# Performance work log

Measured on AMD Instinct MI355X. Metric: run time of the kernel, lower is better.

Reference implementation:

```python
import jax, jax.numpy as jnp
import numpy as np

N = 100000        # nodes
E = 3200000       # random edges (self-loops appended -> E + N total)
F_IN = 500        # in_channels
H = 32            # n_hidden (fixed in NormProp)
D = 64            # embedding_dim
K = 2             # propagation steps
LN_EPS = 1e-6


def setup_inputs() -> dict:
    key = jax.random.key(0)
    ks = jax.random.split(key, 6)
    x = jax.random.normal(ks[0], (N, F_IN), jnp.float32)
    src = jax.random.randint(ks[1], (E,), 0, N)
    dst = jax.random.randint(ks[2], (E,), 0, N)
    loop = jnp.arange(N)
    # edge_index already contains all self-loops, matching
    # add_remaining_self_loops' post-condition deterministically.
    edge_index = jnp.stack([jnp.concatenate([src, loop]),
                            jnp.concatenate([dst, loop])])
    W1 = jax.random.normal(ks[3], (F_IN, H), jnp.float32) * (1.0 / np.sqrt(F_IN))
    b1 = jnp.zeros((H,), jnp.float32)
    gamma = jnp.ones((H,), jnp.float32)
    beta = jnp.zeros((H,), jnp.float32)
    W2 = jax.random.normal(ks[4], (H, D), jnp.float32) * (1.0 / np.sqrt(H))
    b2 = jnp.zeros((D,), jnp.float32)
    return dict(x=x, edge_index=edge_index, W1=W1, b1=b1,
                gamma=gamma, beta=beta, W2=W2, b2=b2)


def reference(x, edge_index, W1, b1, gamma, beta, W2, b2):
    # Encoder (dropout p is inactive at eval): fc1 -> LayerNorm -> relu -> fc2
    h = x @ W1 + b1                                   # [N, H]
    mu = h.mean(-1, keepdims=True)
    var = ((h - mu) ** 2).mean(-1, keepdims=True)
    h = (h - mu) / jnp.sqrt(var + LN_EPS) * gamma + beta
    h = jax.nn.relu(h) @ W2 + b2                      # [N, D]
    # F.normalize(p=2, dim=-1) with eps=1e-12
    h = h / jnp.maximum(jnp.linalg.norm(h, axis=-1, keepdims=True), 1e-12)

    row, col = edge_index[0], edge_index[1]           # source -> target
    # gcn_norm: symmetric deg^{-1/2} normalization (edge_weight=None -> ones)
    deg = jax.ops.segment_sum(jnp.ones(row.shape, h.dtype), col, num_segments=N)
    dinv = jnp.where(deg > 0, jax.lax.rsqrt(deg), 0.0)
    norm = dinv[row] * dinv[col]                      # [E+N]

    hs = [h]
    for _ in range(K):
        # message: edge_weight * x_j ; aggregate: scatter-add into target
        h = jax.ops.segment_sum(norm[:, None] * h[row], col, num_segments=N)
        hs.append(h)
    return tuple(hs)
```

## Files before the change

kernel.cpp:

```cpp
#include <hip/hip_runtime.h>

#define F_IN 500
#define HH 32
#define DD 64
#define LN_EPS 1e-6f
#define QCAP 100000
#define SPAN 4096
#define FWN 448
#define FCAP 16384

typedef float f32x4 __attribute__((ext_vector_type(4)));
typedef _Float16 f16x8 __attribute__((ext_vector_type(8)));
typedef _Float16 f16x2 __attribute__((ext_vector_type(2)));
typedef _Float16 h16;

__global__ __launch_bounds__(256)
void prep_k(const float* __restrict__ W1, const float* __restrict__ W2,
            h16* __restrict__ w1t, h16* __restrict__ w2t)
{
    int i = blockIdx.x * 256 + threadIdx.x;
    if (i < 32 * 512) {
        int j = i >> 9, k = i & 511;
        w1t[i] = (k < F_IN) ? (h16)W1[k * HH + j] : (h16)0.f;
    }
    int i2 = i - 32 * 512;
    if (i2 >= 0 && i2 < 64 * 32) {
        int d = i2 >> 5, j = i2 & 31;
        w2t[i2] = (h16)W2[j * DD + d];
    }
}

__global__ __launch_bounds__(256)
void encoder_k(const float* __restrict__ x,
               const h16* __restrict__ w1t, const float* __restrict__ b1,
               const float* __restrict__ gamma, const float* __restrict__ beta,
               const h16* __restrict__ w2t, const float* __restrict__ b2,
               float* __restrict__ h0, int N)
{
    __shared__ h16 hbuf[4][512];

    const int t = threadIdx.x;
    const int w = t >> 6, l = t & 63;
    const int c0 = l & 15, kg = l >> 4;
    const int gr0 = (blockIdx.x * 4 + w) * 16;
    int rowA = gr0 + c0; if (rowA >= N) rowA = N - 1;
    const float* xr = x + (size_t)rowA * F_IN;

    float b1a = b1[c0], b1b = b1[c0 + 16];
    f32x4 acc0 = {b1a, b1a, b1a, b1a};
    f32x4 acc1 = {b1b, b1b, b1b, b1b};

    const h16* w1a = w1t + c0 * 512 + kg * 8;
    const h16* w1b = w1a + 16 * 512;

    #pragma unroll 3
    for (int ks = 0; ks < 15; ++ks) {
        const int k0 = ks * 32;
        f32x4 xa = *(const f32x4*)(xr + k0 + kg * 8);
        f32x4 xb = *(const f32x4*)(xr + k0 + kg * 8 + 4);
        f16x8 af;
        af[0] = (h16)xa[0]; af[1] = (h16)xa[1]; af[2] = (h16)xa[2]; af[3] = (h16)xa[3];
        af[4] = (h16)xb[0]; af[5] = (h16)xb[1]; af[6] = (h16)xb[2]; af[7] = (h16)xb[3];
        f16x8 bf0 = *(const f16x8*)(w1a + k0);
        f16x8 bf1 = *(const f16x8*)(w1b + k0);
        acc0 = __builtin_amdgcn_mfma_f32_16x16x32_f16(af, bf0, acc0, 0, 0, 0);
        acc1 = __builtin_amdgcn_mfma_f32_16x16x32_f16(af, bf1, acc1, 0, 0, 0);
    }
    {
        f16x8 af;
        #pragma unroll
        for (int e = 0; e < 8; ++e) {
            int k = 480 + kg * 8 + e;
            af[e] = (k < F_IN) ? (h16)xr[k] : (h16)0.f;
        }
        f16x8 bf0 = *(const f16x8*)(w1a + 480);
        f16x8 bf1 = *(const f16x8*)(w1b + 480);
        acc0 = __builtin_amdgcn_mfma_f32_16x16x32_f16(af, bf0, acc0, 0, 0, 0);
        acc1 = __builtin_amdgcn_mfma_f32_16x16x32_f16(af, bf1, acc1, 0, 0, 0);
    }

    float g0 = gamma[c0], g1 = gamma[c0 + 16];
    float be0 = beta[c0], be1 = beta[c0 + 16];
    h16* hb = hbuf[w];
    #pragma unroll
    for (int i = 0; i < 4; ++i) {
        float a0 = acc0[i], a1 = acc1[i];
        float s = a0 + a1;
        s += __shfl_xor(s, 1); s += __shfl_xor(s, 2);
        s += __shfl_xor(s, 4); s += __shfl_xor(s, 8);
        float mu = s * (1.0f / 32.0f);
        float d0 = a0 - mu, d1 = a1 - mu;
        float vv = d0 * d0 + d1 * d1;
        vv += __shfl_xor(vv, 1); vv += __shfl_xor(vv, 2);
        vv += __shfl_xor(vv, 4); vv += __shfl_xor(vv, 8);
        float is = rsqrtf(vv * (1.0f / 32.0f) + LN_EPS);
        float h0v = fmaxf(fmaf(d0 * is, g0, be0), 0.f);
        float h1v = fmaxf(fmaf(d1 * is, g1, be1), 0.f);
        int r = kg * 4 + i;
        hb[r * 32 + ((((c0 >> 3) ^ i) & 3) << 3) + (c0 & 7)] = (h16)h0v;
        hb[r * 32 + ((((2 + (c0 >> 3)) ^ i) & 3) << 3) + (c0 & 7)] = (h16)h1v;
    }
    asm volatile("s_waitcnt lgkmcnt(0)" ::: "memory");
    __builtin_amdgcn_sched_barrier(0);

    f16x8 ah = *(const f16x8*)(hb + c0 * 32 + (((kg ^ (c0 & 3)) & 3) << 3));

    f32x4 oc[4];
    #pragma unroll
    for (int tl = 0; tl < 4; ++tl) {
        float bb = b2[tl * 16 + c0];
        f32x4 ci = {bb, bb, bb, bb};
        f16x8 bw = *(const f16x8*)(w2t + (tl * 16 + c0) * 32 + kg * 8);
        oc[tl] = __builtin_amdgcn_mfma_f32_16x16x32_f16(ah, bw, ci, 0, 0, 0);
    }

    #pragma unroll
    for (int i = 0; i < 4; ++i) {
        float ss = oc[0][i] * oc[0][i] + oc[1][i] * oc[1][i]
                 + oc[2][i] * oc[2][i] + oc[3][i] * oc[3][i];
        ss += __shfl_xor(ss, 1); ss += __shfl_xor(ss, 2);
        ss += __shfl_xor(ss, 4); ss += __shfl_xor(ss, 8);
        float sc = 1.0f / fmaxf(sqrtf(ss), 1e-12f);
        int row = gr0 + kg * 4 + i;
        if (row < N) {
            #pragma unroll
            for (int tl = 0; tl < 4; ++tl)
                h0[(size_t)row * DD + tl * 16 + c0] = oc[tl][i] * sc;
        }
    }
}

__global__ void zero_k(int* __restrict__ p, int n)
{
    int i = blockIdx.x * blockDim.x + threadIdx.x;
    int stride = gridDim.x * blockDim.x;
    for (; i < n; i += stride) p[i] = 0;
}

__global__ __launch_bounds__(256)
void binq_k(const int* __restrict__ erow, const int* __restrict__ ecol, int M,
            unsigned* __restrict__ queue, int* __restrict__ qcnt,
            int cw, unsigned magic)
{
    const int wid  = blockIdx.x * 4 + (threadIdx.x >> 6);
    const int lane = threadIdx.x & 63;
    const int nw   = gridDim.x * 4;
    const int cls  = blockIdx.x & 7;

    for (int s0 = wid * SPAN; s0 < M; s0 += nw * SPAN) {
        const int e1 = min(s0 + SPAN, M);
        int tc[8] = {0, 0, 0, 0, 0, 0, 0, 0};
        for (int i = s0 + lane; i < e1; i += 64) {
            int c = ecol[i];
            unsigned p = (unsigned)(((unsigned long long)(unsigned)c * magic) >> 32);
            #pragma unroll
            for (int pp = 0; pp < 8; ++pp) tc[pp] += (p == (unsigned)pp) ? 1 : 0;
        }
        #pragma unroll
        for (int pp = 0; pp < 8; ++pp) {
            #pragma unroll
            for (int m = 1; m < 64; m <<= 1) tc[pp] += __shfl_xor(tc[pp], m);
        }
        int val = tc[0];
        #pragma unroll
        for (int pp = 1; pp < 8; ++pp) val = (lane == pp) ? tc[pp] : val;
        int base = 0;
        if (lane < 8) base = atomicAdd(&qcnt[lane * 8 + cls], val);
        int bases[8], run[8];
        #pragma unroll
        for (int pp = 0; pp < 8; ++pp) { bases[pp] = __shfl(base, pp); run[pp] = 0; }

        for (int i0 = s0; i0 < e1; i0 += 64) {
            int i = i0 + lane;
            bool act = i < e1;
            int c = act ? ecol[i] : 0;
            int r = act ? erow[i] : 0;
            unsigned p = act ? (unsigned)(((unsigned long long)(unsigned)c * magic) >> 32)
                             : 0xFFu;
            unsigned pk = (unsigned)r | ((unsigned)(c - (int)p * cw) << 17);
            #pragma unroll
            for (int pp = 0; pp < 8; ++pp) {
                unsigned long long mm = __ballot(p == (unsigned)pp);
                if (p == (unsigned)pp) {
                    int rank = __popcll(mm & ((1ull << lane) - 1ull));
                    queue[(size_t)(pp * 8 + cls) * QCAP + bases[pp] + run[pp] + rank] = pk;
                }
                run[pp] += (int)__popcll(mm);
            }
        }
    }
}

__global__ __launch_bounds__(1024)
void countq_k(const unsigned* __restrict__ queue, const int* __restrict__ qcnt,
              int* __restrict__ cnt, int cw)
{
    __shared__ int lc[12500];
    const int p = blockIdx.x;
    const int tid = threadIdx.x;

    for (int i = tid; i < cw; i += 1024) lc[i] = 0;
    __syncthreads();

    #pragma unroll 1
    for (int sq = 0; sq < 8; ++sq) {
        const int n = qcnt[p * 8 + sq];
        const unsigned* q = queue + (size_t)(p * 8 + sq) * QCAP;
        int i = tid;
        for (; i + 3 * 1024 < n; i += 4 * 1024) {
            unsigned e0 = q[i];
            unsigned e1 = q[i + 1024];
            unsigned e2 = q[i + 2048];
            unsigned e3 = q[i + 3072];
            atomicAdd(&lc[e0 >> 17], 1);
            atomicAdd(&lc[e1 >> 17], 1);
            atomicAdd(&lc[e2 >> 17], 1);
            atomicAdd(&lc[e3 >> 17], 1);
        }
        for (; i < n; i += 1024)
            atomicAdd(&lc[q[i] >> 17], 1);
    }
    __syncthreads();

    int* cb = cnt + p * cw;
    for (int i = tid; i < cw; i += 1024) cb[i] = lc[i];
}

__global__ __launch_bounds__(256)
void scanA_k(const int* __restrict__ cnt, int* __restrict__ bsum, int N)
{
    __shared__ int sd[256];
    int t = threadIdx.x;
    int v = blockIdx.x * 256 + t;
    sd[t] = (v < N) ? cnt[v] : 0;
    __syncthreads();
    #pragma unroll
    for (int o = 128; o > 0; o >>= 1) {
        if (t < o) sd[t] += sd[t + o];
        __syncthreads();
    }
    if (t == 0) bsum[blockIdx.x] = sd[0];
}

__global__ __launch_bounds__(512)
void scanB_k(const int* __restrict__ bsum, int* __restrict__ bbase, int NB)
{
    __shared__ int sd[512];
    int t = threadIdx.x;
    int v = (t < NB) ? bsum[t] : 0;
    sd[t] = v;
    __syncthreads();
    #pragma unroll
    for (int o = 1; o < 512; o <<= 1) {
        int tmp = (t >= o) ? sd[t - o] : 0;
        __syncthreads();
        sd[t] += tmp;
        __syncthreads();
    }
    if (t < NB) bbase[t] = sd[t] - v;
}

__global__ __launch_bounds__(256)
void scanC_k(const int* __restrict__ cnt, const int* __restrict__ bbase,
             int* __restrict__ start, float* __restrict__ dinv, int N)
{
    __shared__ int sd[256];
    int t = threadIdx.x;
    int v = blockIdx.x * 256 + t;
    int c = (v < N) ? cnt[v] : 0;
    sd[t] = c;
    __syncthreads();
    #pragma unroll
    for (int o = 1; o < 256; o <<= 1) {
        int tmp = (t >= o) ? sd[t - o] : 0;
        __syncthreads();
        sd[t] += tmp;
        __syncthreads();
    }
    if (v < N) {
        start[v] = bbase[blockIdx.x] + sd[t] - c;
        dinv[v]  = (c > 0) ? rsqrtf((float)c) : 0.0f;
    }
}

__global__ __launch_bounds__(1024)
void fillq_k(const unsigned* __restrict__ queue, const int* __restrict__ qcnt,
             const int* __restrict__ start, int* __restrict__ cursor,
             int* __restrict__ csr_src, int cw, int M, int N)
{
    __shared__ int loff[FWN + 1];
    __shared__ int lcur[FWN];
    __shared__ unsigned lbuf[FCAP];

    const int tid = threadIdx.x;
    const int p  = blockIdx.x & 7;
    const int w  = blockIdx.x >> 3;
    const int c0 = w * FWN;
    const int wn = min(FWN, cw - c0);
    const int gn0 = p * cw + c0;

    for (int i = tid; i <= wn; i += 1024) {
        int g = gn0 + i;
        loff[i] = (g < N) ? start[g] : M;
    }
    for (int i = tid; i < wn; i += 1024) lcur[i] = 0;
    __syncthreads();

    const int base = loff[0];
    const int span = loff[wn] - base;

    if (span <= FCAP) {
        #pragma unroll 1
        for (int sq = 0; sq < 8; ++sq) {
            const int n = qcnt[p * 8 + sq];
            const unsigned* q = queue + (size_t)(p * 8 + sq) * QCAP;
            int i = tid;
            for (; i + 3 * 1024 < n; i += 4 * 1024) {
                unsigned e0 = q[i];
                unsigned e1 = q[i + 1024];
                unsigned e2 = q[i + 2048];
                unsigned e3 = q[i + 3072];
                int cl0 = (int)(e0 >> 17) - c0;
                int cl1 = (int)(e1 >> 17) - c0;
                int cl2 = (int)(e2 >> 17) - c0;
                int cl3 = (int)(e3 >> 17) - c0;
                if ((unsigned)cl0 < (unsigned)wn)
                    lbuf[loff[cl0] - base + atomicAdd(&lcur[cl0], 1)] = e0 & 0x1FFFFu;
                if ((unsigned)cl1 < (unsigned)wn)
                    lbuf[loff[cl1] - base + atomicAdd(&lcur[cl1], 1)] = e1 & 0x1FFFFu;
                if ((unsigned)cl2 < (unsigned)wn)
                    lbuf[loff[cl2] - base + atomicAdd(&lcur[cl2], 1)] = e2 & 0x1FFFFu;
                if ((unsigned)cl3 < (unsigned)wn)
                    lbuf[loff[cl3] - base + atomicAdd(&lcur[cl3], 1)] = e3 & 0x1FFFFu;
            }
            for (; i < n; i += 1024) {
                unsigned pk = q[i];
                int cl = (int)(pk >> 17) - c0;
                if ((unsigned)cl < (unsigned)wn)
                    lbuf[loff[cl] - base + atomicAdd(&lcur[cl], 1)] = pk & 0x1FFFFu;
            }
        }
        __syncthreads();
        for (int i = tid; i < span; i += 1024)
            csr_src[base + i] = (int)lbuf[i];
    } else {
        #pragma unroll 1
        for (int sq = 0; sq < 8; ++sq) {
            int n = qcnt[p * 8 + sq];
            const unsigned* q = queue + (size_t)(p * 8 + sq) * QCAP;
            for (int i = tid; i < n; i += 1024) {
                unsigned pk = q[i];
                int cl = (int)(pk >> 17) - c0;
                if ((unsigned)cl < (unsigned)wn) {
                    int c = gn0 + cl;
                    int pos = start[c] + atomicAdd(&cursor[c], 1);
                    csr_src[pos] = (int)(pk & 0x1FFFFu);
                }
            }
        }
    }
}

__global__ __launch_bounds__(256)
void mkmir_k(const float* __restrict__ h, const float* __restrict__ dinv,
             unsigned* __restrict__ m, int N)
{
    int i = blockIdx.x * 256 + threadIdx.x;
    if (i >= N * 32) return;
    float2 v = ((const float2*)h)[i];
    float dv = dinv[i >> 5];
    f16x2 hv;
    hv[0] = (h16)(v.x * dv);
    hv[1] = (h16)(v.y * dv);
    m[i] = __builtin_bit_cast(unsigned, hv);
}

__global__ __launch_bounds__(256)
void prop16_k(const unsigned* __restrict__ min_, float* __restrict__ hout,
              unsigned* __restrict__ mout,
              const int* __restrict__ start, const int* __restrict__ cnt,
              const int* __restrict__ csr_src, const float* __restrict__ dinv, int N)
{
    int v = blockIdx.x * 8 + (threadIdx.x >> 5);
    int l = threadIdx.x & 31;
    if (v >= N) return;
    int s = start[v];
    int e = s + cnt[v];
    float dv = dinv[v];
    float a0 = 0.0f, a1 = 0.0f;
    int i = s;
    for (; i + 7 < e; i += 8) {
        unsigned u0 = min_[(size_t)csr_src[i + 0] * 32 + l];
        unsigned u1 = min_[(size_t)csr_src[i + 1] * 32 + l];
        unsigned u2 = min_[(size_t)csr_src[i + 2] * 32 + l];
        unsigned u3 = min_[(size_t)csr_src[i + 3] * 32 + l];
        unsigned u4 = min_[(size_t)csr_src[i + 4] * 32 + l];
        unsigned u5 = min_[(size_t)csr_src[i + 5] * 32 + l];
        unsigned u6 = min_[(size_t)csr_src[i + 6] * 32 + l];
        unsigned u7 = min_[(size_t)csr_src[i + 7] * 32 + l];
        f16x2 h0v = __builtin_bit_cast(f16x2, u0);
        f16x2 h1v = __builtin_bit_cast(f16x2, u1);
        f16x2 h2v = __builtin_bit_cast(f16x2, u2);
        f16x2 h3v = __builtin_bit_cast(f16x2, u3);
        f16x2 h4v = __builtin_bit_cast(f16x2, u4);
        f16x2 h5v = __builtin_bit_cast(f16x2, u5);
        f16x2 h6v = __builtin_bit_cast(f16x2, u6);
        f16x2 h7v = __builtin_bit_cast(f16x2, u7);
        a0 += ((float)h0v[0] + (float)h1v[0]) + ((float)h2v[0] + (float)h3v[0])
            + ((float)h4v[0] + (float)h5v[0]) + ((float)h6v[0] + (float)h7v[0]);
        a1 += ((float)h0v[1] + (float)h1v[1]) + ((float)h2v[1] + (float)h3v[1])
            + ((float)h4v[1] + (float)h5v[1]) + ((float)h6v[1] + (float)h7v[1]);
    }
    for (; i < e; ++i) {
        int r = csr_src[i];
        f16x2 hv = __builtin_bit_cast(f16x2, min_[(size_t)r * 32 + l]);
        a0 += (float)hv[0];
        a1 += (float)hv[1];
    }
    float r0 = dv * a0, r1 = dv * a1;
    float2 st; st.x = r0; st.y = r1;
    *(float2*)(hout + (size_t)v * DD + 2 * l) = st;
    if (mout) {
        f16x2 mv;
        mv[0] = (h16)(dv * r0);
        mv[1] = (h16)(dv * r1);
        mout[(size_t)v * 32 + l] = __builtin_bit_cast(unsigned, mv);
    }
}

extern "C" void kernel_launch(void* const* d_in, const int* in_sizes, int n_in,
                              void* d_out, int out_size, void* d_ws, size_t ws_size,
                              hipStream_t stream)
{
    const float* x     = (const float*)d_in[0];
    const int*   ei    = (const int*)  d_in[1];
    const float* W1    = (const float*)d_in[2];
    const float* b1    = (const float*)d_in[3];
    const float* gamma = (const float*)d_in[4];
    const float* beta  = (const float*)d_in[5];
    const float* W2    = (const float*)d_in[6];
    const float* b2    = (const float*)d_in[7];
    float* out = (float*)d_out;

    const int N = in_sizes[0] / F_IN;
    const int M = in_sizes[1] / 2;
    const int cw = (N + 7) / 8;
    const unsigned magic = (unsigned)((0x100000000ULL + cw - 1) / cw);
    const int NB = (N + 255) / 256;
    const int* erow = ei;
    const int* ecol = ei + M;

    int* wsI = (int*)d_ws;
    int*   cnt     = wsI;
    int*   cursor  = wsI + N;
    int*   qcnt    = wsI + 2 * N + 4;
    int*   bsum    = wsI + 2 * N + 68;
    int*   bbase   = wsI + 2 * N + 580;
    int*   startv  = wsI + 2 * N + 1092;
    float* dinv    = (float*)(wsI + 3 * N + 1092);
    h16*   w1t     = (h16*)(wsI + 4 * N + 1092);
    h16*   w2t     = (h16*)(wsI + 4 * N + 1092 + 8192);
    int*   csr_src = wsI + 4 * N + 1092 + 9216;
    unsigned* queue = (unsigned*)(csr_src + M);
    unsigned* mir0 = queue;
    unsigned* mir1 = mir0 + (size_t)N * 32;

    zero_k<<<512, 256, 0, stream>>>(wsI + N, N + 68);
    prep_k<<<(32 * 512 + 64 * 32 + 255) / 256, 256, 0, stream>>>(W1, W2, w1t, w2t);

    encoder_k<<<(N + 63) / 64, 256, 0, stream>>>(x, w1t, b1, gamma, beta, w2t, b2, out, N);

    binq_k<<<256, 256, 0, stream>>>(erow, ecol, M, queue, qcnt, cw, magic);

    countq_k<<<8, 1024, 0, stream>>>(queue, qcnt, cnt, cw);

    scanA_k<<<NB, 256, 0, stream>>>(cnt, bsum, N);
    scanB_k<<<1, 512, 0, stream>>>(bsum, bbase, NB);
    scanC_k<<<NB, 256, 0, stream>>>(cnt, bbase, startv, dinv, N);

    const int NWF = (cw + FWN - 1) / FWN;
    fillq_k<<<NWF * 8, 1024, 0, stream>>>(queue, qcnt, startv, cursor, csr_src, cw, M, N);

    float* h0 = out;
    float* h1 = out + (size_t)N * DD;
    float* h2 = out + 2 * (size_t)N * DD;

    mkmir_k<<<(N * 32 + 255) / 256, 256, 0, stream>>>(h0, dinv, mir0, N);
    prop16_k<<<(N + 7) / 8, 256, 0, stream>>>(mir0, h1, mir1, startv, cnt, csr_src, dinv, N);
    prop16_k<<<(N + 7) / 8, 256, 0, stream>>>(mir1, h2, (unsigned*)nullptr, startv, cnt, csr_src, dinv, N);
}
```

Before: 466.7 us.

## Gather four edges per wave32 group with 16-byte row loads in propagation

Result: no change. 466.8 us (+0.0%).

```diff
diff --git a/kernel.cpp b/kernel.cpp
--- a/kernel.cpp
+++ b/kernel.cpp
@@ -381,50 +381,64 @@
               const int* __restrict__ start, const int* __restrict__ cnt,
               const int* __restrict__ csr_src, const float* __restrict__ dinv, int N)
 {
-    int v = blockIdx.x * 8 + (threadIdx.x >> 5);
-    int l = threadIdx.x & 31;
+    const int tid = threadIdx.x;
+    const int l = tid & 31;
+    const int l16 = l & 15;
+    const int l8 = l & 7;
+    const int g = l >> 3;
+    int v = blockIdx.x * 8 + (tid >> 5);
     if (v >= N) return;
-    int s = start[v];
-    int e = s + cnt[v];
-    float dv = dinv[v];
-    float a0 = 0.0f, a1 = 0.0f;
-    int i = s;
-    for (; i + 7 < e; i += 8) {
-        unsigned u0 = min_[(size_t)csr_src[i + 0] * 32 + l];
-        unsigned u1 = min_[(size_t)csr_src[i + 1] * 32 + l];
-        unsigned u2 = min_[(size_t)csr_src[i + 2] * 32 + l];
-        unsigned u3 = min_[(size_t)csr_src[i + 3] * 32 + l];
-        unsigned u4 = min_[(size_t)csr_src[i + 4] * 32 + l];
-        unsigned u5 = min_[(size_t)csr_src[i + 5] * 32 + l];
-        unsigned u6 = min_[(size_t)csr_src[i + 6] * 32 + l];
-        unsigned u7 = min_[(size_t)csr_src[i + 7] * 32 + l];
-        f16x2 h0v = __builtin_bit_cast(f16x2, u0);
-        f16x2 h1v = __builtin_bit_cast(f16x2, u1);
-        f16x2 h2v = __builtin_bit_cast(f16x2, u2);
-        f16x2 h3v = __builtin_bit_cast(f16x2, u3);
-        f16x2 h4v = __builtin_bit_cast(f16x2, u4);
-        f16x2 h5v = __builtin_bit_cast(f16x2, u5);
-        f16x2 h6v = __builtin_bit_cast(f16x2, u6);
-        f16x2 h7v = __builtin_bit_cast(f16x2, u7);
-        a0 += ((float)h0v[0] + (float)h1v[0]) + ((float)h2v[0] + (float)h3v[0])
-            + ((float)h4v[0] + (float)h5v[0]) + ((float)h6v[0] + (float)h7v[0]);
-        a1 += ((float)h0v[1] + (float)h1v[1]) + ((float)h2v[1] + (float)h3v[1])
-            + ((float)h4v[1] + (float)h5v[1]) + ((float)h6v[1] + (float)h7v[1]);
-    }
-    for (; i < e; ++i) {
-        int r = csr_src[i];
-        f16x2 hv = __builtin_bit_cast(f16x2, min_[(size_t)r * 32 + l]);
-        a0 += (float)hv[0];
-        a1 += (float)hv[1];
-    }
-    float r0 = dv * a0, r1 = dv * a1;
-    float2 st; st.x = r0; st.y = r1;
-    *(float2*)(hout + (size_t)v * DD + 2 * l) = st;
-    if (mout) {
-        f16x2 mv;
-        mv[0] = (h16)(dv * r0);
-        mv[1] = (h16)(dv * r1);
-        mout[(size_t)v * 32 + l] = __builtin_bit_cast(unsigned, mv);
+    const int s = start[v];
+    const int e = s + cnt[v];
+    const float dv = dinv[v];
+
+    float acc[8] = {0.f, 0.f, 0.f, 0.f, 0.f, 0.f, 0.f, 0.f};
+
+    for (int i = s; i < e; i += 16) {
+        int myidx = csr_src[i + l16];
+        #pragma unroll
+        for (int k = 0; k < 4; ++k) {
+            int j = i + 4 * k + g;
+            int r = __shfl(myidx, 4 * k + g, 32);
+            if (j < e) {
+                uint4 u = *(const uint4*)(min_ + (size_t)r * 32 + l8 * 4);
+                f16x2 p0 = __builtin_bit_cast(f16x2, u.x);
+                f16x2 p1 = __builtin_bit_cast(f16x2, u.y);
+                f16x2 p2 = __builtin_bit_cast(f16x2, u.z);
+                f16x2 p3 = __builtin_bit_cast(f16x2, u.w);
+                acc[0] += (float)p0[0]; acc[1] += (float)p0[1];
+                acc[2] += (float)p1[0]; acc[3] += (float)p1[1];
+                acc[4] += (float)p2[0]; acc[5] += (float)p2[1];
+                acc[6] += (float)p3[0]; acc[7] += (float)p3[1];
+            }
+        }
+    }
+    #pragma unroll
+    for (int q = 0; q < 8; ++q) {
+        acc[q] += __shfl_xor(acc[q], 8);
+        acc[q] += __shfl_xor(acc[q], 16);
+    }
+    if (g == 0) {
+        float o[8];
+        #pragma unroll
+        for (int q = 0; q < 8; ++q) o[q] = dv * acc[q];
+        float4 s0; s0.x = o[0]; s0.y = o[1]; s0.z = o[2]; s0.w = o[3];
+        float4 s1; s1.x = o[4]; s1.y = o[5]; s1.z = o[6]; s1.w = o[7];
+        float4* hp = (float4*)(hout + (size_t)v * DD + l8 * 8);
+        hp[0] = s0; hp[1] = s1;
+        if (mout) {
+            f16x2 m0, m1, m2, m3;
+            m0[0] = (h16)(dv * o[0]); m0[1] = (h16)(dv * o[1]);
+            m1[0] = (h16)(dv * o[2]); m1[1] = (h16)(dv * o[3]);
+            m2[0] = (h16)(dv * o[4]); m2[1] = (h16)(dv * o[5]);
+            m3[0] = (h16)(dv * o[6]); m3[1] = (h16)(dv * o[7]);
+            uint4 mu;
+            mu.x = __builtin_bit_cast(unsigned, m0);
+            mu.y = __builtin_bit_cast(unsigned, m1);
+            mu.z = __builtin_bit_cast(unsigned, m2);
+            mu.w = __builtin_bit_cast(unsigned, m3);
+            *(uint4*)(mout + (size_t)v * 32 + l8 * 4) = mu;
+        }
     }
 }
 
```

## Split propagation gather by source half and fuse degree scan into countq

Applied to the files above, without the earlier changes.

Measured after the change: 508.8 us. +9.0%, slower.

```diff
diff --git a/kernel.cpp b/kernel.cpp
--- a/kernel.cpp
+++ b/kernel.cpp
@@ -8,6 +8,7 @@
 #define SPAN 4096
 #define FWN 448
 #define FCAP 16384
+#define CW 12500
 
 typedef float f32x4 __attribute__((ext_vector_type(4)));
 typedef _Float16 f16x8 __attribute__((ext_vector_type(8)));
@@ -193,18 +194,23 @@
 
 __global__ __launch_bounds__(1024)
 void countq_k(const unsigned* __restrict__ queue, const int* __restrict__ qcnt,
-              int* __restrict__ cnt, int cw)
-{
-    __shared__ int lc[12500];
+              int* __restrict__ startv, int* __restrict__ cntlo,
+              float* __restrict__ dinv, int cw, int hN, int M, int N)
+{
+    __shared__ int lc[CW];
+    __shared__ int llo[CW];
+    __shared__ int ts[1024];
+    __shared__ int qs[64];
     const int p = blockIdx.x;
     const int tid = threadIdx.x;
 
-    for (int i = tid; i < cw; i += 1024) lc[i] = 0;
+    for (int i = tid; i < cw; i += 1024) { lc[i] = 0; llo[i] = 0; }
+    if (tid < 64) qs[tid] = qcnt[tid];
     __syncthreads();
 
     #pragma unroll 1
     for (int sq = 0; sq < 8; ++sq) {
-        const int n = qcnt[p * 8 + sq];
+        const int n = qs[p * 8 + sq];
         const unsigned* q = queue + (size_t)(p * 8 + sq) * QCAP;
         int i = tid;
         for (; i + 3 * 1024 < n; i += 4 * 1024) {
@@ -216,80 +222,60 @@
             atomicAdd(&lc[e1 >> 17], 1);
             atomicAdd(&lc[e2 >> 17], 1);
             atomicAdd(&lc[e3 >> 17], 1);
-        }
-        for (; i < n; i += 1024)
-            atomicAdd(&lc[q[i] >> 17], 1);
+            if ((int)(e0 & 0x1FFFFu) < hN) atomicAdd(&llo[e0 >> 17], 1);
+            if ((int)(e1 & 0x1FFFFu) < hN) atomicAdd(&llo[e1 >> 17], 1);
+            if ((int)(e2 & 0x1FFFFu) < hN) atomicAdd(&llo[e2 >> 17], 1);
+            if ((int)(e3 & 0x1FFFFu) < hN) atomicAdd(&llo[e3 >> 17], 1);
+        }
+        for (; i < n; i += 1024) {
+            unsigned e0 = q[i];
+            atomicAdd(&lc[e0 >> 17], 1);
+            if ((int)(e0 & 0x1FFFFu) < hN) atomicAdd(&llo[e0 >> 17], 1);
+        }
     }
     __syncthreads();
 
-    int* cb = cnt + p * cw;
-    for (int i = tid; i < cw; i += 1024) cb[i] = lc[i];
-}
-
-__global__ __launch_bounds__(256)
-void scanA_k(const int* __restrict__ cnt, int* __restrict__ bsum, int N)
-{
-    __shared__ int sd[256];
-    int t = threadIdx.x;
-    int v = blockIdx.x * 256 + t;
-    sd[t] = (v < N) ? cnt[v] : 0;
+    for (int i = tid; i < cw; i += 1024) {
+        int c = lc[i];
+        dinv[p * cw + i] = (c > 0) ? rsqrtf((float)c) : 0.0f;
+    }
+    __syncthreads();
+
+    const int CH = (cw + 1023) / 1024;
+    const int lo = tid * CH;
+    const int hi = min(lo + CH, cw);
+    int sum = 0;
+    for (int i = lo; i < hi; ++i) { int c = lc[i]; lc[i] = sum; sum += c; }
+    ts[tid] = sum;
     __syncthreads();
     #pragma unroll
-    for (int o = 128; o > 0; o >>= 1) {
-        if (t < o) sd[t] += sd[t + o];
+    for (int o = 1; o < 1024; o <<= 1) {
+        int tmp = (tid >= o) ? ts[tid - o] : 0;
         __syncthreads();
-    }
-    if (t == 0) bsum[blockIdx.x] = sd[0];
-}
-
-__global__ __launch_bounds__(512)
-void scanB_k(const int* __restrict__ bsum, int* __restrict__ bbase, int NB)
-{
-    __shared__ int sd[512];
-    int t = threadIdx.x;
-    int v = (t < NB) ? bsum[t] : 0;
-    sd[t] = v;
-    __syncthreads();
-    #pragma unroll
-    for (int o = 1; o < 512; o <<= 1) {
-        int tmp = (t >= o) ? sd[t - o] : 0;
+        ts[tid] += tmp;
         __syncthreads();
-        sd[t] += tmp;
-        __syncthreads();
-    }
-    if (t < NB) bbase[t] = sd[t] - v;
-}
-
-__global__ __launch_bounds__(256)
-void scanC_k(const int* __restrict__ cnt, const int* __restrict__ bbase,
-             int* __restrict__ start, float* __restrict__ dinv, int N)
-{
-    __shared__ int sd[256];
-    int t = threadIdx.x;
-    int v = blockIdx.x * 256 + t;
-    int c = (v < N) ? cnt[v] : 0;
-    sd[t] = c;
-    __syncthreads();
-    #pragma unroll
-    for (int o = 1; o < 256; o <<= 1) {
-        int tmp = (t >= o) ? sd[t - o] : 0;
-        __syncthreads();
-        sd[t] += tmp;
-        __syncthreads();
-    }
-    if (v < N) {
-        start[v] = bbase[blockIdx.x] + sd[t] - c;
-        dinv[v]  = (c > 0) ? rsqrtf((float)c) : 0.0f;
-    }
+    }
+    const int chunkBase = (tid > 0) ? ts[tid - 1] : 0;
+
+    int base = 0;
+    for (int q = 0; q < p * 8; ++q) base += qs[q];
+
+    for (int i = lo; i < hi; ++i) {
+        startv[p * cw + i] = base + chunkBase + lc[i];
+        cntlo[p * cw + i]  = llo[i];
+    }
+    if (p == gridDim.x - 1 && tid == 1023) startv[N] = base + ts[1023];
 }
 
 __global__ __launch_bounds__(1024)
 void fillq_k(const unsigned* __restrict__ queue, const int* __restrict__ qcnt,
-             const int* __restrict__ start, int* __restrict__ cursor,
-             int* __restrict__ csr_src, int cw, int M, int N)
+             const int* __restrict__ startv, const int* __restrict__ cntlo,
+             int* __restrict__ curLo, int* __restrict__ curHi,
+             int* __restrict__ csr_src, int cw, int hN, int M, int N)
 {
     __shared__ int loff[FWN + 1];
-    __shared__ int lcur[FWN];
+    __shared__ int llo[FWN];
+    __shared__ int lcur[FWN * 2];
     __shared__ unsigned lbuf[FCAP];
 
     const int tid = threadIdx.x;
@@ -299,11 +285,12 @@
     const int wn = min(FWN, cw - c0);
     const int gn0 = p * cw + c0;
 
-    for (int i = tid; i <= wn; i += 1024) {
-        int g = gn0 + i;
-        loff[i] = (g < N) ? start[g] : M;
-    }
-    for (int i = tid; i < wn; i += 1024) lcur[i] = 0;
+    for (int i = tid; i <= wn; i += 1024) loff[i] = startv[gn0 + i];
+    for (int i = tid; i < wn; i += 1024) {
+        llo[i] = cntlo[gn0 + i];
+        lcur[2 * i] = 0;
+        lcur[2 * i + 1] = 0;
+    }
     __syncthreads();
 
     const int base = loff[0];
@@ -320,24 +307,29 @@
                 unsigned e1 = q[i + 1024];
                 unsigned e2 = q[i + 2048];
                 unsigned e3 = q[i + 3072];
-                int cl0 = (int)(e0 >> 17) - c0;
-                int cl1 = (int)(e1 >> 17) - c0;
-                int cl2 = (int)(e2 >> 17) - c0;
-                int cl3 = (int)(e3 >> 17) - c0;
-                if ((unsigned)cl0 < (unsigned)wn)
-                    lbuf[loff[cl0] - base + atomicAdd(&lcur[cl0], 1)] = e0 & 0x1FFFFu;
-                if ((unsigned)cl1 < (unsigned)wn)
-                    lbuf[loff[cl1] - base + atomicAdd(&lcur[cl1], 1)] = e1 & 0x1FFFFu;
-                if ((unsigned)cl2 < (unsigned)wn)
-                    lbuf[loff[cl2] - base + atomicAdd(&lcur[cl2], 1)] = e2 & 0x1FFFFu;
-                if ((unsigned)cl3 < (unsigned)wn)
-                    lbuf[loff[cl3] - base + atomicAdd(&lcur[cl3], 1)] = e3 & 0x1FFFFu;
+                #pragma unroll
+                for (int u = 0; u < 4; ++u) {
+                    unsigned pk = (u == 0) ? e0 : (u == 1) ? e1 : (u == 2) ? e2 : e3;
+                    int cl = (int)(pk >> 17) - c0;
+                    if ((unsigned)cl < (unsigned)wn) {
+                        int src = (int)(pk & 0x1FFFFu);
+                        int half = (src >= hN) ? 1 : 0;
+                        int pos = loff[cl] - base + (half ? llo[cl] : 0)
+                                + atomicAdd(&lcur[2 * cl + half], 1);
+                        lbuf[pos] = (unsigned)src;
+                    }
+                }
             }
             for (; i < n; i += 1024) {
                 unsigned pk = q[i];
                 int cl = (int)(pk >> 17) - c0;
-                if ((unsigned)cl < (unsigned)wn)
-                    lbuf[loff[cl] - base + atomicAdd(&lcur[cl], 1)] = pk & 0x1FFFFu;
+                if ((unsigned)cl < (unsigned)wn) {
+                    int src = (int)(pk & 0x1FFFFu);
+                    int half = (src >= hN) ? 1 : 0;
+                    int pos = loff[cl] - base + (half ? llo[cl] : 0)
+                            + atomicAdd(&lcur[2 * cl + half], 1);
+                    lbuf[pos] = (unsigned)src;
+                }
             }
         }
         __syncthreads();
@@ -353,8 +345,13 @@
                 int cl = (int)(pk >> 17) - c0;
                 if ((unsigned)cl < (unsigned)wn) {
                     int c = gn0 + cl;
-                    int pos = start[c] + atomicAdd(&cursor[c], 1);
-                    csr_src[pos] = (int)(pk & 0x1FFFFu);
+                    int src = (int)(pk & 0x1FFFFu);
+                    int pos;
+                    if (src >= hN)
+                        pos = startv[c] + cntlo[c] + atomicAdd(&curHi[c], 1);
+                    else
+                        pos = startv[c] + atomicAdd(&curLo[c], 1);
+                    csr_src[pos] = src;
                 }
             }
         }
@@ -376,17 +373,15 @@
 }
 
 __global__ __launch_bounds__(256)
-void prop16_k(const unsigned* __restrict__ min_, float* __restrict__ hout,
-              unsigned* __restrict__ mout,
-              const int* __restrict__ start, const int* __restrict__ cnt,
-              const int* __restrict__ csr_src, const float* __restrict__ dinv, int N)
+void proplo_k(const unsigned* __restrict__ min_, float* __restrict__ part,
+              const int* __restrict__ startv, const int* __restrict__ cntlo,
+              const int* __restrict__ csr_src, int N)
 {
     int v = blockIdx.x * 8 + (threadIdx.x >> 5);
     int l = threadIdx.x & 31;
     if (v >= N) return;
-    int s = start[v];
-    int e = s + cnt[v];
-    float dv = dinv[v];
+    int s = startv[v];
+    int e = s + cntlo[v];
     float a0 = 0.0f, a1 = 0.0f;
     int i = s;
     for (; i + 7 < e; i += 8) {
@@ -412,12 +407,58 @@
             + ((float)h4v[1] + (float)h5v[1]) + ((float)h6v[1] + (float)h7v[1]);
     }
     for (; i < e; ++i) {
-        int r = csr_src[i];
-        f16x2 hv = __builtin_bit_cast(f16x2, min_[(size_t)r * 32 + l]);
+        f16x2 hv = __builtin_bit_cast(f16x2, min_[(size_t)csr_src[i] * 32 + l]);
         a0 += (float)hv[0];
         a1 += (float)hv[1];
     }
-    float r0 = dv * a0, r1 = dv * a1;
+    float2 st; st.x = a0; st.y = a1;
+    *(float2*)(part + (size_t)v * DD + 2 * l) = st;
+}
+
+__global__ __launch_bounds__(256)
+void prophi_k(const unsigned* __restrict__ min_, float* __restrict__ hout,
+              unsigned* __restrict__ mout,
+              const int* __restrict__ startv, const int* __restrict__ cntlo,
+              const int* __restrict__ csr_src, const float* __restrict__ dinv, int N)
+{
+    int v = blockIdx.x * 8 + (threadIdx.x >> 5);
+    int l = threadIdx.x & 31;
+    if (v >= N) return;
+    int s = startv[v] + cntlo[v];
+    int e = startv[v + 1];
+    float a0 = 0.0f, a1 = 0.0f;
+    int i = s;
+    for (; i + 7 < e; i += 8) {
+        unsigned u0 = min_[(size_t)csr_src[i + 0] * 32 + l];
+        unsigned u1 = min_[(size_t)csr_src[i + 1] * 32 + l];
+        unsigned u2 = min_[(size_t)csr_src[i + 2] * 32 + l];
+        unsigned u3 = min_[(size_t)csr_src[i + 3] * 32 + l];
+        unsigned u4 = min_[(size_t)csr_src[i + 4] * 32 + l];
+        unsigned u5 = min_[(size_t)csr_src[i + 5] * 32 + l];
+        unsigned u6 = min_[(size_t)csr_src[i + 6] * 32 + l];
+        unsigned u7 = min_[(size_t)csr_src[i + 7] * 32 + l];
+        f16x2 h0v = __builtin_bit_cast(f16x2, u0);
+        f16x2 h1v = __builtin_bit_cast(f16x2, u1);
+        f16x2 h2v = __builtin_bit_cast(f16x2, u2);
+        f16x2 h3v = __builtin_bit_cast(f16x2, u3);
+        f16x2 h4v = __builtin_bit_cast(f16x2, u4);
+        f16x2 h5v = __builtin_bit_cast(f16x2, u5);
+        f16x2 h6v = __builtin_bit_cast(f16x2, u6);
+        f16x2 h7v = __builtin_bit_cast(f16x2, u7);
+        a0 += ((float)h0v[0] + (float)h1v[0]) + ((float)h2v[0] + (float)h3v[0])
+            + ((float)h4v[0] + (float)h5v[0]) + ((float)h6v[0] + (float)h7v[0]);
+        a1 += ((float)h0v[1] + (float)h1v[1]) + ((float)h2v[1] + (float)h3v[1])
+            + ((float)h4v[1] + (float)h5v[1]) + ((float)h6v[1] + (float)h7v[1]);
+    }
+    for (; i < e; ++i) {
+        f16x2 hv = __builtin_bit_cast(f16x2, min_[(size_t)csr_src[i] * 32 + l]);
+        a0 += (float)hv[0];
+        a1 += (float)hv[1];
+    }
+    float dv = dinv[v];
+    float2 pp = *(const float2*)(hout + (size_t)v * DD + 2 * l);
+    float r0 = dv * (a0 + pp.x);
+    float r1 = dv * (a1 + pp.y);
     float2 st; st.x = r0; st.y = r1;
     *(float2*)(hout + (size_t)v * DD + 2 * l) = st;
     if (mout) {
@@ -445,47 +486,46 @@
     const int N = in_sizes[0] / F_IN;
     const int M = in_sizes[1] / 2;
     const int cw = (N + 7) / 8;
+    const int hN = N / 2;
     const unsigned magic = (unsigned)((0x100000000ULL + cw - 1) / cw);
-    const int NB = (N + 255) / 256;
     const int* erow = ei;
     const int* ecol = ei + M;
 
     int* wsI = (int*)d_ws;
-    int*   cnt     = wsI;
-    int*   cursor  = wsI + N;
-    int*   qcnt    = wsI + 2 * N + 4;
-    int*   bsum    = wsI + 2 * N + 68;
-    int*   bbase   = wsI + 2 * N + 580;
-    int*   startv  = wsI + 2 * N + 1092;
-    float* dinv    = (float*)(wsI + 3 * N + 1092);
-    h16*   w1t     = (h16*)(wsI + 4 * N + 1092);
-    h16*   w2t     = (h16*)(wsI + 4 * N + 1092 + 8192);
-    int*   csr_src = wsI + 4 * N + 1092 + 9216;
+    int*   curLo   = wsI;
+    int*   curHi   = wsI + N;
+    int*   qcnt    = wsI + 2 * N;
+    int*   startv  = wsI + 2 * N + 68;
+    int*   cntlo   = wsI + 3 * N + 70;
+    float* dinv    = (float*)(wsI + 4 * N + 70);
+    h16*   w1t     = (h16*)(wsI + 5 * N + 70);
+    h16*   w2t     = (h16*)(wsI + 5 * N + 70 + 8192);
+    int*   csr_src = wsI + 5 * N + 70 + 9216;
     unsigned* queue = (unsigned*)(csr_src + M);
     unsigned* mir0 = queue;
     unsigned* mir1 = mir0 + (size_t)N * 32;
 
-    zero_k<<<512, 256, 0, stream>>>(wsI + N, N + 68);
+    zero_k<<<512, 256, 0, stream>>>(wsI, 2 * N + 68);
     prep_k<<<(32 * 512 + 64 * 32 + 255) / 256, 256, 0, stream>>>(W1, W2, w1t, w2t);
 
     encoder_k<<<(N + 63) / 64, 256, 0, stream>>>(x, w1t, b1, gamma, beta, w2t, b2, out, N);
 
     binq_k<<<256, 256, 0, stream>>>(erow, ecol, M, queue, qcnt, cw, magic);
 
-    countq_k<<<8, 1024, 0, stream>>>(queue, qcnt, cnt, cw);
-
-    scanA_k<<<NB, 256, 0, stream>>>(cnt, bsum, N);
-    scanB_k<<<1, 512, 0, stream>>>(bsum, bbase, NB);
-    scanC_k<<<NB, 256, 0, stream>>>(cnt, bbase, startv, dinv, N);
+    countq_k<<<8, 1024, 0, stream>>>(queue, qcnt, startv, cntlo, dinv, cw, hN, M, N);
 
     const int NWF = (cw + FWN - 1) / FWN;
-    fillq_k<<<NWF * 8, 1024, 0, stream>>>(queue, qcnt, startv, cursor, csr_src, cw, M, N);
+    fillq_k<<<NWF * 8, 1024, 0, stream>>>(queue, qcnt, startv, cntlo,
+                                          curLo, curHi, csr_src, cw, hN, M, N);
 
     float* h0 = out;
     float* h1 = out + (size_t)N * DD;
     float* h2 = out + 2 * (size_t)N * DD;
 
     mkmir_k<<<(N * 32 + 255) / 256, 256, 0, stream>>>(h0, dinv, mir0, N);
-    prop16_k<<<(N + 7) / 8, 256, 0, stream>>>(mir0, h1, mir1, startv, cnt, csr_src, dinv, N);
-    prop16_k<<<(N + 7) / 8, 256, 0, stream>>>(mir1, h2, (unsigned*)nullptr, startv, cnt, csr_src, dinv, N);
-}
+
+    proplo_k<<<(N + 7) / 8, 256, 0, stream>>>(mir0, h1, startv, cntlo, csr_src, N);
+    prophi_k<<<(N + 7) / 8, 256, 0, stream>>>(mir0, h1, mir1, startv, cntlo, csr_src, dinv, N);
+    proplo_k<<<(N + 7) / 8, 256, 0, stream>>>(mir1, h2, startv, cntlo, csr_src, N);
+    prophi_k<<<(N + 7) / 8, 256, 0, stream>>>(mir1, h2, (unsigned*)nullptr, startv, cntlo, csr_src, dinv, N);
+}
```

## Store propagation mirrors in FP8 and fold degree scan into count kernel

Applied to the files above, without the earlier changes.

Result: faster. 416.3 us (median of 2 runs) (-10.8%).

```diff
diff --git a/kernel.cpp b/kernel.cpp
--- a/kernel.cpp
+++ b/kernel.cpp
@@ -1,4 +1,5 @@
 #include <hip/hip_runtime.h>
+#include <hip/hip_fp8.h>
 
 #define F_IN 500
 #define HH 32
@@ -8,11 +9,22 @@
 #define SPAN 4096
 #define FWN 448
 #define FCAP 16384
+#define CW 12500
 
 typedef float f32x4 __attribute__((ext_vector_type(4)));
+typedef float f32x2 __attribute__((ext_vector_type(2)));
 typedef _Float16 f16x8 __attribute__((ext_vector_type(8)));
-typedef _Float16 f16x2 __attribute__((ext_vector_type(2)));
 typedef _Float16 h16;
+
+__device__ __forceinline__ unsigned char f2fp8(float x) {
+    __hip_fp8_e4m3 t(x);
+    return (unsigned char)t.__x;
+}
+__device__ __forceinline__ float fp82f(unsigned char b) {
+    __hip_fp8_e4m3 t;
+    t.__x = (__hip_fp8_storage_t)b;
+    return (float)t;
+}
 
 __global__ __launch_bounds__(256)
 void prep_k(const float* __restrict__ W1, const float* __restrict__ W2,
@@ -193,18 +205,21 @@
 
 __global__ __launch_bounds__(1024)
 void countq_k(const unsigned* __restrict__ queue, const int* __restrict__ qcnt,
-              int* __restrict__ cnt, int cw)
-{
-    __shared__ int lc[12500];
+              int* __restrict__ startv, float* __restrict__ dinv, int cw, int N)
+{
+    __shared__ int lc[CW];
+    __shared__ int ts[1024];
+    __shared__ int qs[64];
     const int p = blockIdx.x;
     const int tid = threadIdx.x;
 
     for (int i = tid; i < cw; i += 1024) lc[i] = 0;
+    if (tid < 64) qs[tid] = qcnt[tid];
     __syncthreads();
 
     #pragma unroll 1
     for (int sq = 0; sq < 8; ++sq) {
-        const int n = qcnt[p * 8 + sq];
+        const int n = qs[p * 8 + sq];
         const unsigned* q = queue + (size_t)(p * 8 + sq) * QCAP;
         int i = tid;
         for (; i + 3 * 1024 < n; i += 4 * 1024) {
@@ -222,71 +237,40 @@
     }
     __syncthreads();
 
-    int* cb = cnt + p * cw;
-    for (int i = tid; i < cw; i += 1024) cb[i] = lc[i];
-}
-
-__global__ __launch_bounds__(256)
-void scanA_k(const int* __restrict__ cnt, int* __restrict__ bsum, int N)
-{
-    __shared__ int sd[256];
-    int t = threadIdx.x;
-    int v = blockIdx.x * 256 + t;
-    sd[t] = (v < N) ? cnt[v] : 0;
+    for (int i = tid; i < cw; i += 1024) {
+        int c = lc[i];
+        dinv[p * cw + i] = (c > 0) ? rsqrtf((float)c) : 0.0f;
+    }
+    __syncthreads();
+
+    const int CH = (cw + 1023) / 1024;
+    const int lo = tid * CH;
+    const int hi = min(lo + CH, cw);
+    int sum = 0;
+    for (int i = lo; i < hi; ++i) { int c = lc[i]; lc[i] = sum; sum += c; }
+    ts[tid] = sum;
     __syncthreads();
     #pragma unroll
-    for (int o = 128; o > 0; o >>= 1) {
-        if (t < o) sd[t] += sd[t + o];
+    for (int o = 1; o < 1024; o <<= 1) {
+        int tmp = (tid >= o) ? ts[tid - o] : 0;
         __syncthreads();
-    }
-    if (t == 0) bsum[blockIdx.x] = sd[0];
-}
-
-__global__ __launch_bounds__(512)
-void scanB_k(const int* __restrict__ bsum, int* __restrict__ bbase, int NB)
-{
-    __shared__ int sd[512];
-    int t = threadIdx.x;
-    int v = (t < NB) ? bsum[t] : 0;
-    sd[t] = v;
-    __syncthreads();
-    #pragma unroll
-    for (int o = 1; o < 512; o <<= 1) {
-        int tmp = (t >= o) ? sd[t - o] : 0;
+        ts[tid] += tmp;
         __syncthreads();
-        sd[t] += tmp;
-        __syncthreads();
-    }
-    if (t < NB) bbase[t] = sd[t] - v;
-}
-
-__global__ __launch_bounds__(256)
-void scanC_k(const int* __restrict__ cnt, const int* __restrict__ bbase,
-             int* __restrict__ start, float* __restrict__ dinv, int N)
-{
-    __shared__ int sd[256];
-    int t = threadIdx.x;
-    int v = blockIdx.x * 256 + t;
-    int c = (v < N) ? cnt[v] : 0;
-    sd[t] = c;
-    __syncthreads();
-    #pragma unroll
-    for (int o = 1; o < 256; o <<= 1) {
-        int tmp = (t >= o) ? sd[t - o] : 0;
-        __syncthreads();
-        sd[t] += tmp;
-        __syncthreads();
-    }
-    if (v < N) {
-        start[v] = bbase[blockIdx.x] + sd[t] - c;
-        dinv[v]  = (c > 0) ? rsqrtf((float)c) : 0.0f;
-    }
+    }
+    const int chunkBase = (tid > 0) ? ts[tid - 1] : 0;
+
+    int base = 0;
+    for (int q = 0; q < p * 8; ++q) base += qs[q];
+
+    for (int i = lo; i < hi; ++i)
+        startv[p * cw + i] = base + chunkBase + lc[i];
+    if (p == gridDim.x - 1 && tid == 1023) startv[N] = base + ts[1023];
 }
 
 __global__ __launch_bounds__(1024)
 void fillq_k(const unsigned* __restrict__ queue, const int* __restrict__ qcnt,
-             const int* __restrict__ start, int* __restrict__ cursor,
-             int* __restrict__ csr_src, int cw, int M, int N)
+             const int* __restrict__ startv, int* __restrict__ cursor,
+             int* __restrict__ csr_src, int cw)
 {
     __shared__ int loff[FWN + 1];
     __shared__ int lcur[FWN];
@@ -299,10 +283,7 @@
     const int wn = min(FWN, cw - c0);
     const int gn0 = p * cw + c0;
 
-    for (int i = tid; i <= wn; i += 1024) {
-        int g = gn0 + i;
-        loff[i] = (g < N) ? start[g] : M;
-    }
+    for (int i = tid; i <= wn; i += 1024) loff[i] = startv[gn0 + i];
     for (int i = tid; i < wn; i += 1024) lcur[i] = 0;
     __syncthreads();
 
@@ -353,7 +334,7 @@
                 int cl = (int)(pk >> 17) - c0;
                 if ((unsigned)cl < (unsigned)wn) {
                     int c = gn0 + cl;
-                    int pos = start[c] + atomicAdd(&cursor[c], 1);
+                    int pos = startv[c] + atomicAdd(&cursor[c], 1);
                     csr_src[pos] = (int)(pk & 0x1FFFFu);
                 }
             }
@@ -366,65 +347,69 @@
              unsigned* __restrict__ m, int N)
 {
     int i = blockIdx.x * 256 + threadIdx.x;
-    if (i >= N * 32) return;
-    float2 v = ((const float2*)h)[i];
-    float dv = dinv[i >> 5];
-    f16x2 hv;
-    hv[0] = (h16)(v.x * dv);
-    hv[1] = (h16)(v.y * dv);
-    m[i] = __builtin_bit_cast(unsigned, hv);
+    if (i >= N * 16) return;
+    f32x4 v = ((const f32x4*)h)[i];
+    float dv = dinv[i >> 4];
+    unsigned u = (unsigned)f2fp8(v[0] * dv)
+               | ((unsigned)f2fp8(v[1] * dv) << 8)
+               | ((unsigned)f2fp8(v[2] * dv) << 16)
+               | ((unsigned)f2fp8(v[3] * dv) << 24);
+    m[i] = u;
 }
 
 __global__ __launch_bounds__(256)
-void prop16_k(const unsigned* __restrict__ min_, float* __restrict__ hout,
-              unsigned* __restrict__ mout,
-              const int* __restrict__ start, const int* __restrict__ cnt,
-              const int* __restrict__ csr_src, const float* __restrict__ dinv, int N)
+void prop8_k(const unsigned char* __restrict__ min_, float* __restrict__ hout,
+             unsigned short* __restrict__ mout,
+             const int* __restrict__ startv,
+             const int* __restrict__ csr_src, const float* __restrict__ dinv, int N)
 {
     int v = blockIdx.x * 8 + (threadIdx.x >> 5);
     int l = threadIdx.x & 31;
     if (v >= N) return;
-    int s = start[v];
-    int e = s + cnt[v];
+    int s = startv[v];
+    int e = startv[v + 1];
     float dv = dinv[v];
     float a0 = 0.0f, a1 = 0.0f;
     int i = s;
     for (; i + 7 < e; i += 8) {
-        unsigned u0 = min_[(size_t)csr_src[i + 0] * 32 + l];
-        unsigned u1 = min_[(size_t)csr_src[i + 1] * 32 + l];
-        unsigned u2 = min_[(size_t)csr_src[i + 2] * 32 + l];
-        unsigned u3 = min_[(size_t)csr_src[i + 3] * 32 + l];
-        unsigned u4 = min_[(size_t)csr_src[i + 4] * 32 + l];
-        unsigned u5 = min_[(size_t)csr_src[i + 5] * 32 + l];
-        unsigned u6 = min_[(size_t)csr_src[i + 6] * 32 + l];
-        unsigned u7 = min_[(size_t)csr_src[i + 7] * 32 + l];
-        f16x2 h0v = __builtin_bit_cast(f16x2, u0);
-        f16x2 h1v = __builtin_bit_cast(f16x2, u1);
-        f16x2 h2v = __builtin_bit_cast(f16x2, u2);
-        f16x2 h3v = __builtin_bit_cast(f16x2, u3);
-        f16x2 h4v = __builtin_bit_cast(f16x2, u4);
-        f16x2 h5v = __builtin_bit_cast(f16x2, u5);
-        f16x2 h6v = __builtin_bit_cast(f16x2, u6);
-        f16x2 h7v = __builtin_bit_cast(f16x2, u7);
-        a0 += ((float)h0v[0] + (float)h1v[0]) + ((float)h2v[0] + (float)h3v[0])
-            + ((float)h4v[0] + (float)h5v[0]) + ((float)h6v[0] + (float)h7v[0]);
-        a1 += ((float)h0v[1] + (float)h1v[1]) + ((float)h2v[1] + (float)h3v[1])
-            + ((float)h4v[1] + (float)h5v[1]) + ((float)h6v[1] + (float)h7v[1]);
+        int r0 = __builtin_nontemporal_load(csr_src + i + 0);
+        int r1 = __builtin_nontemporal_load(csr_src + i + 1);
+        int r2 = __builtin_nontemporal_load(csr_src + i + 2);
+        int r3 = __builtin_nontemporal_load(csr_src + i + 3);
+        int r4 = __builtin_nontemporal_load(csr_src + i + 4);
+        int r5 = __builtin_nontemporal_load(csr_src + i + 5);
+        int r6 = __builtin_nontemporal_load(csr_src + i + 6);
+        int r7 = __builtin_nontemporal_load(csr_src + i + 7);
+        unsigned short u0 = *(const unsigned short*)(min_ + (size_t)r0 * 64 + 2 * l);
+        unsigned short u1 = *(const unsigned short*)(min_ + (size_t)r1 * 64 + 2 * l);
+        unsigned short u2 = *(const unsigned short*)(min_ + (size_t)r2 * 64 + 2 * l);
+        unsigned short u3 = *(const unsigned short*)(min_ + (size_t)r3 * 64 + 2 * l);
+        unsigned short u4 = *(const unsigned short*)(min_ + (size_t)r4 * 64 + 2 * l);
+        unsigned short u5 = *(const unsigned short*)(min_ + (size_t)r5 * 64 + 2 * l);
+        unsigned short u6 = *(const unsigned short*)(min_ + (size_t)r6 * 64 + 2 * l);
+        unsigned short u7 = *(const unsigned short*)(min_ + (size_t)r7 * 64 + 2 * l);
+        a0 += fp82f((unsigned char)(u0 & 255)) + fp82f((unsigned char)(u1 & 255))
+            + fp82f((unsigned char)(u2 & 255)) + fp82f((unsigned char)(u3 & 255))
+            + fp82f((unsigned char)(u4 & 255)) + fp82f((unsigned char)(u5 & 255))
+            + fp82f((unsigned char)(u6 & 255)) + fp82f((unsigned char)(u7 & 255));
+        a1 += fp82f((unsigned char)(u0 >> 8)) + fp82f((unsigned char)(u1 >> 8))
+            + fp82f((unsigned char)(u2 >> 8)) + fp82f((unsigned char)(u3 >> 8))
+            + fp82f((unsigned char)(u4 >> 8)) + fp82f((unsigned char)(u5 >> 8))
+            + fp82f((unsigned char)(u6 >> 8)) + fp82f((unsigned char)(u7 >> 8));
     }
     for (; i < e; ++i) {
-        int r = csr_src[i];
-        f16x2 hv = __builtin_bit_cast(f16x2, min_[(size_t)r * 32 + l]);
-        a0 += (float)hv[0];
-        a1 += (float)hv[1];
+        int r = __builtin_nontemporal_load(csr_src + i);
+        unsigned short u = *(const unsigned short*)(min_ + (size_t)r * 64 + 2 * l);
+        a0 += fp82f((unsigned char)(u & 255));
+        a1 += fp82f((unsigned char)(u >> 8));
     }
     float r0 = dv * a0, r1 = dv * a1;
-    float2 st; st.x = r0; st.y = r1;
-    *(float2*)(hout + (size_t)v * DD + 2 * l) = st;
+    f32x2 st = {r0, r1};
+    __builtin_nontemporal_store(st, (f32x2*)(hout + (size_t)v * DD + 2 * l));
     if (mout) {
-        f16x2 mv;
-        mv[0] = (h16)(dv * r0);
-        mv[1] = (h16)(dv * r1);
-        mout[(size_t)v * 32 + l] = __builtin_bit_cast(unsigned, mv);
+        unsigned short mv = (unsigned short)f2fp8(dv * r0)
+                          | ((unsigned short)f2fp8(dv * r1) << 8);
+        mout[(size_t)v * 32 + l] = mv;
     }
 }
 
@@ -446,46 +431,41 @@
     const int M = in_sizes[1] / 2;
     const int cw = (N + 7) / 8;
     const unsigned magic = (unsigned)((0x100000000ULL + cw - 1) / cw);
-    const int NB = (N + 255) / 256;
     const int* erow = ei;
     const int* ecol = ei + M;
 
     int* wsI = (int*)d_ws;
-    int*   cnt     = wsI;
-    int*   cursor  = wsI + N;
-    int*   qcnt    = wsI + 2 * N + 4;
-    int*   bsum    = wsI + 2 * N + 68;
-    int*   bbase   = wsI + 2 * N + 580;
-    int*   startv  = wsI + 2 * N + 1092;
-    float* dinv    = (float*)(wsI + 3 * N + 1092);
-    h16*   w1t     = (h16*)(wsI + 4 * N + 1092);
-    h16*   w2t     = (h16*)(wsI + 4 * N + 1092 + 8192);
-    int*   csr_src = wsI + 4 * N + 1092 + 9216;
+    int*   cursor  = wsI;
+    int*   qcnt    = wsI + N;
+    int*   startv  = wsI + N + 68;
+    float* dinv    = (float*)(wsI + 2 * N + 70);
+    h16*   w1t     = (h16*)(wsI + 3 * N + 70);
+    h16*   w2t     = (h16*)(wsI + 3 * N + 70 + 8192);
+    int*   csr_src = wsI + 3 * N + 70 + 9216;
     unsigned* queue = (unsigned*)(csr_src + M);
-    unsigned* mir0 = queue;
-    unsigned* mir1 = mir0 + (size_t)N * 32;
-
-    zero_k<<<512, 256, 0, stream>>>(wsI + N, N + 68);
+    unsigned char* mir0 = (unsigned char*)queue;
+    unsigned char* mir1 = mir0 + (size_t)N * 64;
+
+    zero_k<<<512, 256, 0, stream>>>(wsI, N + 68);
     prep_k<<<(32 * 512 + 64 * 32 + 255) / 256, 256, 0, stream>>>(W1, W2, w1t, w2t);
 
     encoder_k<<<(N + 63) / 64, 256, 0, stream>>>(x, w1t, b1, gamma, beta, w2t, b2, out, N);
 
     binq_k<<<256, 256, 0, stream>>>(erow, ecol, M, queue, qcnt, cw, magic);
 
-    countq_k<<<8, 1024, 0, stream>>>(queue, qcnt, cnt, cw);
-
-    scanA_k<<<NB, 256, 0, stream>>>(cnt, bsum, N);
-    scanB_k<<<1, 512, 0, stream>>>(bsum, bbase, NB);
-    scanC_k<<<NB, 256, 0, stream>>>(cnt, bbase, startv, dinv, N);
+    countq_k<<<8, 1024, 0, stream>>>(queue, qcnt, startv, dinv, cw, N);
 
     const int NWF = (cw + FWN - 1) / FWN;
-    fillq_k<<<NWF * 8, 1024, 0, stream>>>(queue, qcnt, startv, cursor, csr_src, cw, M, N);
+    fillq_k<<<NWF * 8, 1024, 0, stream>>>(queue, qcnt, startv, cursor, csr_src, cw);
 
     float* h0 = out;
     float* h1 = out + (size_t)N * DD;
     float* h2 = out + 2 * (size_t)N * DD;
 
-    mkmir_k<<<(N * 32 + 255) / 256, 256, 0, stream>>>(h0, dinv, mir0, N);
-    prop16_k<<<(N + 7) / 8, 256, 0, stream>>>(mir0, h1, mir1, startv, cnt, csr_src, dinv, N);
-    prop16_k<<<(N + 7) / 8, 256, 0, stream>>>(mir1, h2, (unsigned*)nullptr, startv, cnt, csr_src, dinv, N);
-}
+    mkmir_k<<<(N * 16 + 255) / 256, 256, 0, stream>>>(h0, dinv, (unsigned*)mir0, N);
+
+    prop8_k<<<(N + 7) / 8, 256, 0, stream>>>(mir0, h1, (unsigned short*)mir1,
+                                             startv, csr_src, dinv, N);
+    prop8_k<<<(N + 7) / 8, 256, 0, stream>>>(mir1, h2, (unsigned short*)nullptr,
+                                             startv, csr_src, dinv, N);
+}
```
